# Optimization experiments

Hardware: AMD Instinct MI355X
Metric: run time of the kernel (lower is better)

## Reference

```python
import jax, jax.numpy as jnp
import numpy as np

B, N, DIM = 8, 2048, 1024
HEADS, CB_DIM, CB_SIZE = 8, 64, 1024
CB_IN = HEADS * CB_DIM  # 512


def setup_inputs() -> dict:
    key = jax.random.key(0)
    ks = jax.random.split(key, 4)
    x = jax.random.normal(ks[0], (B, N, DIM), dtype=jnp.float32)
    W_in = jax.random.normal(ks[1], (DIM, CB_IN), dtype=jnp.float32) * (DIM ** -0.5)
    b_in = jnp.zeros((CB_IN,), dtype=jnp.float32)
    W_out = jax.random.normal(ks[2], (CB_IN, DIM), dtype=jnp.float32) * (CB_IN ** -0.5)
    b_out = jnp.zeros((DIM,), dtype=jnp.float32)
    embed = jax.random.normal(ks[3], (CB_SIZE, CB_DIM), dtype=jnp.float32)
    return {"x": x, "W_in": W_in, "b_in": b_in, "W_out": W_out, "b_out": b_out, "embed": embed}


def reference(x, W_in, b_in, W_out, b_out, embed):
    # project_in: [B, N, DIM] -> [B, N, HEADS*CB_DIM]
    h = jnp.einsum("bnd,de->bne", x, W_in) + b_in
    # multi-head split, shared codebook: 'b n (h d) -> (b h) n d' view as [B, N, H, d]
    hx = h.reshape(B, N, HEADS, CB_DIM)
    # euclidean nearest neighbor: argmin ||hx - e||^2 == argmax (2 hx.e - ||e||^2)
    dots = jnp.einsum("bnhd,cd->bnhc", hx, embed)          # [B, N, H, C]
    e_sq = jnp.sum(embed * embed, axis=-1)                    # [C]
    scores = 2.0 * dots - e_sq                                 # monotone in -dist
    embed_ind = jnp.argmax(scores, axis=-1)                    # [B, N, H] int
    quantize = embed[embed_ind]                                # [B, N, H, d] gather
    # merge heads and project_out
    q = quantize.reshape(B, N, CB_IN)
    out = jnp.einsum("bne,ed->bnd", q, W_out) + b_out          # [B, N, DIM]
    return out, embed_ind
```

## Files before the change

### kernel.cpp

```cpp
#include <hip/hip_runtime.h>

#define B_      8
#define N_      2048
#define DIM_    1024
#define HEADS_  8
#define CBD_    64
#define CBS_    1024
#define CBIN_   512
#define M_      (B_*N_)
#define M2_     (M_*HEADS_)

#define MARGIN 0.02f
#define XSTR   40

typedef unsigned short ushort_t;
typedef __attribute__((ext_vector_type(8))) short short8;
typedef __attribute__((ext_vector_type(4))) float f32x4;

__device__ inline ushort_t f2bf(float f) {
    unsigned int u = __builtin_bit_cast(unsigned int, f);
    unsigned int r = u + 0x7FFFu + ((u >> 16) & 1u);
    return (ushort_t)(r >> 16);
}
__device__ inline float bf2f(ushort_t h) {
    unsigned int u = ((unsigned int)h) << 16;
    return __builtin_bit_cast(float, u);
}
__device__ inline f32x4 mfma_bf16(short8 a, short8 b, f32x4 c) {
    return __builtin_amdgcn_mfma_f32_16x16x32_bf16(a, b, c, 0, 0, 0);
}
__device__ inline void store4u(ushort_t* p, ushort_t a, ushort_t b, ushort_t c, ushort_t d) {
    uint2 u;
    u.x = (unsigned int)a | ((unsigned int)b << 16);
    u.y = (unsigned int)c | ((unsigned int)d << 16);
    *(uint2*)p = u;
}
__device__ inline void split3(float f, ushort_t& s1, ushort_t& s2, ushort_t& s3) {
    s1 = f2bf(f);
    float r = f - bf2f(s1);
    s2 = f2bf(r);
    float r2 = r - bf2f(s2);
    s3 = f2bf(r2);
}
__device__ inline void async_cp16(void* lds, const void* g) {
    __builtin_amdgcn_global_load_lds(
        (const __attribute__((address_space(1))) unsigned int*)g,
        (__attribute__((address_space(3))) unsigned int*)lds, 16, 0, 0);
}

__global__ __launch_bounds__(256) void esq_kernel(const float* __restrict__ embed,
                                                  float* __restrict__ esq) {
    int c = blockIdx.x * 256 + threadIdx.x;
    if (c < CBS_) {
        const float* e = embed + (size_t)c * CBD_;
        float s = 0.f;
#pragma unroll
        for (int d = 0; d < CBD_; ++d) s += e[d] * e[d];
        esq[c] = s;
    }
}

__global__ __launch_bounds__(256) void split_embed(const float* __restrict__ embed,
                                                   ushort_t* __restrict__ hi,
                                                   ushort_t* __restrict__ lo) {
    int i = blockIdx.x * 256 + threadIdx.x;
    int code = i >> 6, d = i & 63;
    int dst = code * 64 + ((((d >> 3) ^ (code & 7)) << 3) | (d & 7));
    float f = embed[i];
    ushort_t hh = f2bf(f);
    hi[dst] = hh;
    lo[dst] = f2bf(f - bf2f(hh));
}

__global__ __launch_bounds__(256) void transposeW(const float* __restrict__ W,
                                                  ushort_t* __restrict__ WT) {
    __shared__ ushort_t t[64][65];
    const int tid = threadIdx.x;
    const int n0 = blockIdx.x * 64, k0 = blockIdx.y * 64;
#pragma unroll
    for (int s = 0; s < 16; ++s) {
        int i = s * 256 + tid;
        int r = i >> 6, c = i & 63;
        t[r][c] = f2bf(W[(size_t)(k0 + r) * DIM_ + n0 + c]);
    }
    __syncthreads();
#pragma unroll
    for (int s = 0; s < 16; ++s) {
        int i = s * 256 + tid;
        int r = i >> 6, c = i & 63;
        WT[(size_t)(n0 + r) * CBIN_ + k0 + c] = t[c][r];
    }
}

__global__ __launch_bounds__(256) void split_WinT(const float* __restrict__ W,
                                                  ushort_t* __restrict__ W1T,
                                                  ushort_t* __restrict__ W2T,
                                                  ushort_t* __restrict__ W3T) {
    __shared__ ushort_t t1[64][65];
    __shared__ ushort_t t2[64][65];
    __shared__ ushort_t t3[64][65];
    const int tid = threadIdx.x;
    const int n0 = blockIdx.x * 64, k0 = blockIdx.y * 64;
#pragma unroll
    for (int s = 0; s < 16; ++s) {
        int i = s * 256 + tid;
        int r = i >> 6, c = i & 63;
        float f = W[(size_t)(k0 + r) * CBIN_ + n0 + c];
        split3(f, t1[r][c], t2[r][c], t3[r][c]);
    }
    __syncthreads();
#pragma unroll
    for (int s = 0; s < 16; ++s) {
        int i = s * 256 + tid;
        int r = i >> 6, c = i & 63;
        size_t o = (size_t)(n0 + r) * DIM_ + k0 + c;
        W1T[o] = t1[c][r];
        W2T[o] = t2[c][r];
        W3T[o] = t3[c][r];
    }
}

__global__ __launch_bounds__(256) void gemm_in_x6(const float* __restrict__ x,
                                                  const ushort_t* __restrict__ W1T,
                                                  const ushort_t* __restrict__ W2T,
                                                  const ushort_t* __restrict__ W3T,
                                                  const float* __restrict__ bias,
                                                  float* __restrict__ C) {
    __shared__ ushort_t A1[128 * XSTR];
    __shared__ ushort_t A2[128 * XSTR];
    __shared__ ushort_t A3[128 * XSTR];
    __shared__ ushort_t B1[128 * XSTR];
    __shared__ ushort_t B2[128 * XSTR];
    __shared__ ushort_t B3[128 * XSTR];

    const int tid  = threadIdx.x;
    const int lane = tid & 63;
    const int w    = tid >> 6;
    const int quad = lane >> 4;
    const int col  = lane & 15;
    const int m0   = blockIdx.y * 128;
    const int n0   = blockIdx.x * 128;
    const int wm   = (w & 1) * 64;
    const int wn   = (w >> 1) * 64;

    f32x4 acc[4][4];
#pragma unroll
    for (int rt = 0; rt < 4; ++rt)
#pragma unroll
        for (int ct = 0; ct < 4; ++ct) acc[rt][ct] = (f32x4){0.f, 0.f, 0.f, 0.f};

    for (int k0 = 0; k0 < DIM_; k0 += 32) {
        __syncthreads();
#pragma unroll
        for (int s = 0; s < 4; ++s) {
            int f = s * 256 + tid;
            int row = f >> 3, qq = f & 7;
            float4 v = *(const float4*)(x + (size_t)(m0 + row) * DIM_ + k0 + qq * 4);
            float vv[4] = {v.x, v.y, v.z, v.w};
            ushort_t p1[4], p2[4], p3[4];
#pragma unroll
            for (int j = 0; j < 4; ++j) split3(vv[j], p1[j], p2[j], p3[j]);
            int base = row * XSTR + qq * 4;
            store4u(&A1[base], p1[0], p1[1], p1[2], p1[3]);
            store4u(&A2[base], p2[0], p2[1], p2[2], p2[3]);
            store4u(&A3[base], p3[0], p3[1], p3[2], p3[3]);
        }
#pragma unroll
        for (int s = 0; s < 2; ++s) {
            int f = s * 256 + tid;
            int row = f >> 2, g = f & 3;
            size_t go = (size_t)(n0 + row) * DIM_ + k0 + g * 8;
            int lo = row * XSTR + g * 8;
            *(uint4*)&B1[lo] = *(const uint4*)(W1T + go);
            *(uint4*)&B2[lo] = *(const uint4*)(W2T + go);
            *(uint4*)&B3[lo] = *(const uint4*)(W3T + go);
        }
        __syncthreads();

        short8 a1[4], a2[4], a3[4], b1[4], b2[4], b3[4];
#pragma unroll
        for (int rt = 0; rt < 4; ++rt) {
            int o = (wm + rt * 16 + col) * XSTR + quad * 8;
            a1[rt] = *(const short8*)&A1[o];
            a2[rt] = *(const short8*)&A2[o];
            a3[rt] = *(const short8*)&A3[o];
        }
#pragma unroll
        for (int ct = 0; ct < 4; ++ct) {
            int o = (wn + ct * 16 + col) * XSTR + quad * 8;
            b1[ct] = *(const short8*)&B1[o];
            b2[ct] = *(const short8*)&B2[o];
            b3[ct] = *(const short8*)&B3[o];
        }
#define COMBO(AP, BP)                                                   \
        _Pragma("unroll")                                               \
        for (int ct = 0; ct < 4; ++ct)                                  \
            _Pragma("unroll")                                           \
            for (int rt = 0; rt < 4; ++rt)                              \
                acc[rt][ct] = mfma_bf16(AP[rt], BP[ct], acc[rt][ct]);
        COMBO(a1, b1); COMBO(a1, b2); COMBO(a2, b1);
        COMBO(a2, b2); COMBO(a1, b3); COMBO(a3, b1);
#undef COMBO
    }

#pragma unroll
    for (int ct = 0; ct < 4; ++ct) {
        int gc = n0 + wn + ct * 16 + col;
        float bb = bias[gc];
#pragma unroll
        for (int rt = 0; rt < 4; ++rt) {
#pragma unroll
            for (int reg = 0; reg < 4; ++reg) {
                int gr = m0 + wm + rt * 16 + quad * 4 + reg;
                C[(size_t)gr * CBIN_ + gc] = acc[rt][ct][reg] + bb;
            }
        }
    }
}

__global__ __launch_bounds__(256, 4) void argmax2(const float* __restrict__ h,
                                                  const ushort_t* __restrict__ ehswz,
                                                  const ushort_t* __restrict__ elswz,
                                                  const float* __restrict__ esq,
                                                  const float* __restrict__ embed,
                                                  float* __restrict__ outIdxF,
                                                  int* __restrict__ outIdxI) {
    __shared__ ushort_t EB[2][2][4096];
    __shared__ float    ESQ[CBS_];
    __shared__ int BIDX[128];
    __shared__ int FLAG[128];
    __shared__ int NFLAG;

    const int tid  = threadIdx.x;
    const int lane = tid & 63;
    const int w    = tid >> 6;
    const int quad = lane >> 4;
    const int col  = lane & 15;
    const int r0   = blockIdx.x * 128;

    if (tid == 0) NFLAG = 0;
    *(float4*)&ESQ[tid * 4] = *(const float4*)(esq + tid * 4);

    short8 AH[2][2], AL[2][2];
#pragma unroll
    for (int rt = 0; rt < 2; ++rt) {
        const float* hp = h + (size_t)(r0 + w * 32 + rt * 16 + col) * 64 + quad * 8;
#pragma unroll
        for (int ks = 0; ks < 2; ++ks) {
            float4 u0 = *(const float4*)(hp + ks * 32);
            float4 u1 = *(const float4*)(hp + ks * 32 + 4);
            float vv[8] = {u0.x, u0.y, u0.z, u0.w, u1.x, u1.y, u1.z, u1.w};
            short8 hh, ll;
#pragma unroll
            for (int j = 0; j < 8; ++j) {
                ushort_t hi = f2bf(vv[j]);
                hh[j] = (short)hi;
                ll[j] = (short)f2bf(vv[j] - bf2f(hi));
            }
            AH[rt][ks] = hh;
            AL[rt][ks] = ll;
        }
    }

#define STAGE(ch, b)                                                          \
    do {                                                                      \
        int eo = (ch) * 4096 + tid * 8;                                       \
        int wo = w * 512;                                                     \
        async_cp16(&EB[b][0][wo],        ehswz + eo);                         \
        async_cp16(&EB[b][0][2048 + wo], ehswz + eo + 2048);                  \
        async_cp16(&EB[b][1][wo],        elswz + eo);                         \
        async_cp16(&EB[b][1][2048 + wo], elswz + eo + 2048);                  \
    } while (0)

    STAGE(0, 0);

    float v1[8], v2[8];
    int   i1[8];
#pragma unroll
    for (int s = 0; s < 8; ++s) { v1[s] = -3.4e38f; v2[s] = -3.4e38f; i1[s] = 0; }

    __syncthreads();

    int cur = 0;
    for (int ch = 0; ch < 16; ++ch) {
        if (ch < 15) STAGE(ch + 1, cur ^ 1);
#pragma unroll
        for (int ct = 0; ct < 4; ++ct) {
            const int lc = ct * 16 + col;
            const int x7 = col & 7;
            const int o0 = lc * 64 + (((quad)     ^ x7) << 3);
            const int o1 = lc * 64 + (((quad + 4) ^ x7) << 3);
            short8 BH0 = *(const short8*)&EB[cur][0][o0];
            short8 BH1 = *(const short8*)&EB[cur][0][o1];
            short8 BL0 = *(const short8*)&EB[cur][1][o0];
            short8 BL1 = *(const short8*)&EB[cur][1][o1];
            const int code = ch * 64 + lc;
            float eq = ESQ[code];
#pragma unroll
            for (int rt = 0; rt < 2; ++rt) {
                f32x4 acc = {0.f, 0.f, 0.f, 0.f};
                acc = mfma_bf16(AH[rt][0], BH0, acc);
                acc = mfma_bf16(AH[rt][1], BH1, acc);
                acc = mfma_bf16(AH[rt][0], BL0, acc);
                acc = mfma_bf16(AH[rt][1], BL1, acc);
                acc = mfma_bf16(AL[rt][0], BH0, acc);
                acc = mfma_bf16(AL[rt][1], BH1, acc);
#pragma unroll
                for (int reg = 0; reg < 4; ++reg) {
                    const int st = rt * 4 + reg;
                    float sc = fmaf(2.f, acc[reg], -eq);
                    v2[st] = __builtin_amdgcn_fmed3f(sc, v1[st], v2[st]);
                    bool gt = sc > v1[st];
                    v1[st] = fmaxf(v1[st], sc);
                    i1[st] = gt ? code : i1[st];
                }
            }
        }
        __syncthreads();
        cur ^= 1;
    }
#undef STAGE

#pragma unroll
    for (int st = 0; st < 8; ++st) {
#pragma unroll
        for (int m = 1; m <= 8; m <<= 1) {
            float ov1 = __shfl_xor(v1[st], m);
            int   oi1 = __shfl_xor(i1[st], m);
            float ov2 = __shfl_xor(v2[st], m);
            float losr = fminf(v1[st], ov1);
            v2[st] = fmaxf(fmaxf(v2[st], ov2), losr);
            bool take = (ov1 > v1[st]) || (ov1 == v1[st] && oi1 < i1[st]);
            v1[st] = take ? ov1 : v1[st];
            i1[st] = take ? oi1 : i1[st];
        }
        if (col == 0) {
            int rt = st >> 2, reg = st & 3;
            int row_l = w * 32 + rt * 16 + quad * 4 + reg;
            BIDX[row_l] = i1[st];
            if (v1[st] - v2[st] < MARGIN) {
                int p = atomicAdd(&NFLAG, 1);
                FLAG[p] = row_l;
            }
        }
    }
    __syncthreads();

    int nf = NFLAG;
    for (int i = w; i < nf; i += 4) {
        int row_l = FLAG[i];
        const float* hr = h + (size_t)(r0 + row_l) * 64;
        float accf[16];
#pragma unroll
        for (int j = 0; j < 16; ++j) accf[j] = 0.f;
        for (int d4 = 0; d4 < 16; ++d4) {
            float4 hv = *(const float4*)(hr + d4 * 4);
#pragma unroll
            for (int j = 0; j < 16; ++j) {
                int c = lane + 64 * j;
                float4 ev = *(const float4*)(embed + (size_t)c * 64 + d4 * 4);
                accf[j] += hv.x * ev.x + hv.y * ev.y + hv.z * ev.z + hv.w * ev.w;
            }
        }
        float best = -3.4e38f; int bi = 0;
#pragma unroll
        for (int j = 0; j < 16; ++j) {
            int c = lane + 64 * j;
            float sc = 2.f * accf[j] - ESQ[c];
            if (sc > best) { best = sc; bi = c; }
        }
#pragma unroll
        for (int m = 1; m <= 32; m <<= 1) {
            float ob = __shfl_xor(best, m);
            int  obi = __shfl_xor(bi, m);
            if (ob > best || (ob == best && obi < bi)) { best = ob; bi = obi; }
        }
        if (lane == 0) BIDX[row_l] = bi;
    }
    __syncthreads();

    if (tid < 128) {
        int b = BIDX[tid];
        outIdxF[r0 + tid] = (float)b;
        outIdxI[r0 + tid] = b;
    }
}

__global__ __launch_bounds__(256) void gemm_out_bf16(const ushort_t* __restrict__ ehswz,
                                                     const int* __restrict__ idx,
                                                     const ushort_t* __restrict__ WbfT,
                                                     const float* __restrict__ bias,
                                                     float* __restrict__ C) {
    __shared__ ushort_t Qs[128 * 72];
    __shared__ ushort_t Ws[128 * 72];
    __shared__ int idxs[128 * HEADS_];

    const int tid  = threadIdx.x;
    const int lane = tid & 63;
    const int w    = tid >> 6;
    const int quad = lane >> 4;
    const int col  = lane & 15;
    const int m0   = blockIdx.y * 128;
    const int n0   = blockIdx.x * 128;
    const int wm   = (w & 1) * 64;
    const int wn   = (w >> 1) * 64;

#pragma unroll
    for (int s = 0; s < 4; ++s) {
        int f = s * 256 + tid;
        idxs[f] = idx[(size_t)m0 * HEADS_ + f];
    }

    f32x4 acc[4][4];
#pragma unroll
    for (int rt = 0; rt < 4; ++rt)
#pragma unroll
        for (int ct = 0; ct < 4; ++ct) acc[rt][ct] = (f32x4){0.f, 0.f, 0.f, 0.f};

    for (int k0 = 0; k0 < CBIN_; k0 += 64) {
        __syncthreads();
        int head = k0 >> 6;
#pragma unroll
        for (int s = 0; s < 4; ++s) {
            int f = s * 256 + tid;
            int row = f >> 3, g = f & 7;
            int e = idxs[row * HEADS_ + head];
            *(uint4*)&Qs[row * 72 + g * 8] =
                *(const uint4*)(ehswz + (size_t)e * 64 + ((g ^ (e & 7)) << 3));
            *(uint4*)&Ws[row * 72 + g * 8] =
                *(const uint4*)(WbfT + (size_t)(n0 + row) * CBIN_ + k0 + g * 8);
        }
        __syncthreads();
#pragma unroll
        for (int ks = 0; ks < 2; ++ks) {
            short8 a[4], b[4];
#pragma unroll
            for (int rt = 0; rt < 4; ++rt)
                a[rt] = *(const short8*)&Qs[(wm + rt * 16 + col) * 72 + ks * 32 + quad * 8];
#pragma unroll
            for (int ct = 0; ct < 4; ++ct)
                b[ct] = *(const short8*)&Ws[(wn + ct * 16 + col) * 72 + ks * 32 + quad * 8];
#pragma unroll
            for (int rt = 0; rt < 4; ++rt)
#pragma unroll
                for (int ct = 0; ct < 4; ++ct)
                    acc[rt][ct] = mfma_bf16(a[rt], b[ct], acc[rt][ct]);
        }
    }

#pragma unroll
    for (int ct = 0; ct < 4; ++ct) {
        int gc = n0 + wn + ct * 16 + col;
        float bb = bias[gc];
#pragma unroll
        for (int rt = 0; rt < 4; ++rt) {
#pragma unroll
            for (int reg = 0; reg < 4; ++reg) {
                int gr = m0 + wm + rt * 16 + quad * 4 + reg;
                C[(size_t)gr * DIM_ + gc] = acc[rt][ct][reg] + bb;
            }
        }
    }
}

extern "C" void kernel_launch(void* const* d_in, const int* in_sizes, int n_in,
                              void* d_out, int out_size, void* d_ws, size_t ws_size,
                              hipStream_t stream) {
    const float* x     = (const float*)d_in[0];
    const float* W_in  = (const float*)d_in[1];
    const float* b_in  = (const float*)d_in[2];
    const float* W_out = (const float*)d_in[3];
    const float* b_out = (const float*)d_in[4];
    const float* embed = (const float*)d_in[5];

    float* out     = (float*)d_out;
    float* outIdxF = out + (size_t)M_ * DIM_;

    char* ws = (char*)d_ws;
    float*    h     = (float*)ws;
    int*      idxI  = (int*)(ws + 33554432);
    float*    esq   = (float*)(ws + 34078720);
    ushort_t* ehswz = (ushort_t*)(ws + 34082816);
    ushort_t* elswz = (ushort_t*)(ws + 34213888);
    ushort_t* WbfT  = (ushort_t*)(ws + 34344960);
    ushort_t* W1T   = (ushort_t*)(ws + 35393536);
    ushort_t* W2T   = (ushort_t*)(ws + 36442112);
    ushort_t* W3T   = (ushort_t*)(ws + 37490688);

    esq_kernel<<<dim3(CBS_ / 256), dim3(256), 0, stream>>>(embed, esq);
    split_embed<<<dim3(CBS_ * CBD_ / 256), dim3(256), 0, stream>>>(embed, ehswz, elswz);
    transposeW<<<dim3(DIM_ / 64, CBIN_ / 64), dim3(256), 0, stream>>>(W_out, WbfT);
    split_WinT<<<dim3(CBIN_ / 64, DIM_ / 64), dim3(256), 0, stream>>>(W_in, W1T, W2T, W3T);
    gemm_in_x6<<<dim3(CBIN_ / 128, M_ / 128), dim3(256), 0, stream>>>(x, W1T, W2T, W3T,
                                                                      b_in, h);
    argmax2<<<dim3(M2_ / 128), dim3(256), 0, stream>>>(h, ehswz, elswz, esq, embed,
                                                       outIdxF, idxI);
    gemm_out_bf16<<<dim3(DIM_ / 128, M_ / 128), dim3(256), 0, stream>>>(ehswz, idxI, WbfT,
                                                                        b_out, out);
}
```

Baseline: 369.9 us.

## Split MFMA chain into two accumulators, fold codebook norm into init, swizzle gemm_in blocks

The codebook scoring loop now runs two independent MFMA accumulator chains instead of one serial chain of six. The -0.5*||e||^2 term is folded into the initial accumulator value, so the score scale is halved and the recheck margin is halved to match. Separately, the input projection GEMM remaps block indices so eight consecutive blocks share the same weight column tile across different row tiles, aiming for better L2 reuse. The two-chain split shortens the MFMA dependency latency but uses more accumulator registers.

```diff
diff --git a/kernel.cpp b/kernel.cpp
--- a/kernel.cpp
+++ b/kernel.cpp
@@ -10,7 +10,7 @@
 #define M_      (B_*N_)
 #define M2_     (M_*HEADS_)
 
-#define MARGIN 0.02f
+#define MARGIN_H 0.01f
 #define XSTR   40
 
 typedef unsigned short ushort_t;
@@ -138,8 +138,13 @@
     const int w    = tid >> 6;
     const int quad = lane >> 4;
     const int col  = lane & 15;
-    const int m0   = blockIdx.y * 128;
-    const int n0   = blockIdx.x * 128;
+
+    const int slot   = blockIdx.y * 4 + blockIdx.x;
+    const int g      = slot & 7;
+    const int t      = slot >> 3;
+    const int m0     = (g + 8 * (t >> 2)) * 128;
+    const int n0     = (t & 3) * 128;
+
     const int wm   = (w & 1) * 64;
     const int wn   = (w >> 1) * 64;
 
@@ -168,9 +173,9 @@
 #pragma unroll
         for (int s = 0; s < 2; ++s) {
             int f = s * 256 + tid;
-            int row = f >> 2, g = f & 3;
-            size_t go = (size_t)(n0 + row) * DIM_ + k0 + g * 8;
-            int lo = row * XSTR + g * 8;
+            int row = f >> 2, g2 = f & 3;
+            size_t go = (size_t)(n0 + row) * DIM_ + k0 + g2 * 8;
+            int lo = row * XSTR + g2 * 8;
             *(uint4*)&B1[lo] = *(const uint4*)(W1T + go);
             *(uint4*)&B2[lo] = *(const uint4*)(W2T + go);
             *(uint4*)&B3[lo] = *(const uint4*)(W3T + go);
@@ -295,20 +300,21 @@
             short8 BL0 = *(const short8*)&EB[cur][1][o0];
             short8 BL1 = *(const short8*)&EB[cur][1][o1];
             const int code = ch * 64 + lc;
-            float eq = ESQ[code];
+            const float neqh = -0.5f * ESQ[code];
 #pragma unroll
             for (int rt = 0; rt < 2; ++rt) {
-                f32x4 acc = {0.f, 0.f, 0.f, 0.f};
-                acc = mfma_bf16(AH[rt][0], BH0, acc);
-                acc = mfma_bf16(AH[rt][1], BH1, acc);
-                acc = mfma_bf16(AH[rt][0], BL0, acc);
-                acc = mfma_bf16(AH[rt][1], BL1, acc);
-                acc = mfma_bf16(AL[rt][0], BH0, acc);
-                acc = mfma_bf16(AL[rt][1], BH1, acc);
+                f32x4 c1 = {neqh, neqh, neqh, neqh};
+                f32x4 c2 = {0.f, 0.f, 0.f, 0.f};
+                c1 = mfma_bf16(AH[rt][0], BH0, c1);
+                c2 = mfma_bf16(AH[rt][1], BH1, c2);
+                c1 = mfma_bf16(AH[rt][0], BL0, c1);
+                c2 = mfma_bf16(AH[rt][1], BL1, c2);
+                c1 = mfma_bf16(AL[rt][0], BH0, c1);
+                c2 = mfma_bf16(AL[rt][1], BH1, c2);
 #pragma unroll
                 for (int reg = 0; reg < 4; ++reg) {
                     const int st = rt * 4 + reg;
-                    float sc = fmaf(2.f, acc[reg], -eq);
+                    float sc = c1[reg] + c2[reg];
                     v2[st] = __builtin_amdgcn_fmed3f(sc, v1[st], v2[st]);
                     bool gt = sc > v1[st];
                     v1[st] = fmaxf(v1[st], sc);
@@ -338,7 +344,7 @@
             int rt = st >> 2, reg = st & 3;
             int row_l = w * 32 + rt * 16 + quad * 4 + reg;
             BIDX[row_l] = i1[st];
-            if (v1[st] - v2[st] < MARGIN) {
+            if (v1[st] - v2[st] < MARGIN_H) {
                 int p = atomicAdd(&NFLAG, 1);
                 FLAG[p] = row_l;
             }
```

After: 450.2 us. +21.7%, slower.
